# Kernel tuning notes

Measured on AMD Instinct MI355X. Metric: run time of the kernel, lower is better.

## Reference

```python
import jax, jax.numpy as jnp
import numpy as np

D_MODEL = 256
D_STATE = 256
BATCH = 32
SEQ = 4096
RMIN, RMAX = 0.9, 0.999
NEG_SLOPE = 0.01
EPS = 1e-5


def layer_norm(x, w=None, b=None):
    m = jnp.mean(x, axis=-1, keepdims=True)
    v = jnp.var(x, axis=-1, keepdims=True)
    y = (x - m) * jax.lax.rsqrt(v + EPS)
    if w is not None:
        y = y * w + b
    return y


def leaky_relu(x):
    return jnp.where(x >= 0, x, NEG_SLOPE * x)


def setup_inputs() -> dict:
    key = jax.random.key(0)
    ks = jax.random.split(key, 12)
    x = jax.random.normal(ks[0], (BATCH, SEQ, D_MODEL), dtype=jnp.float32)
    # LRU ring init: |lambda| uniform in [rmin, rmax], phase uniform in [0, 2pi]
    u1 = jax.random.uniform(ks[1], (D_STATE,), dtype=jnp.float32)
    u2 = jax.random.uniform(ks[2], (D_STATE,), dtype=jnp.float32)
    nu_log = jnp.log(-0.5 * jnp.log(u1 * (RMAX**2 - RMIN**2) + RMIN**2))
    theta_log = jnp.log(2 * jnp.pi * u2)
    lam_mod = jnp.exp(-jnp.exp(nu_log))
    gamma_log = jnp.log(jnp.sqrt(1.0 - lam_mod**2))
    B_re = jax.random.normal(ks[3], (D_STATE, D_MODEL)) / np.sqrt(2 * D_MODEL)
    B_im = jax.random.normal(ks[4], (D_STATE, D_MODEL)) / np.sqrt(2 * D_MODEL)
    C_re = jax.random.normal(ks[5], (D_STATE, D_STATE)) / np.sqrt(D_STATE)
    C_im = jax.random.normal(ks[6], (D_STATE, D_STATE)) / np.sqrt(D_STATE)
    Dm = jax.random.normal(ks[7], (D_STATE, D_MODEL)) / np.sqrt(D_MODEL)
    Wl = jax.random.normal(ks[8], (D_MODEL, D_STATE)) / np.sqrt(D_STATE)
    bl = jax.random.normal(ks[9], (D_MODEL,)) * 0.02
    Wr = jax.random.normal(ks[10], (D_MODEL, D_STATE)) / np.sqrt(D_STATE)
    br = jax.random.normal(ks[11], (D_MODEL,)) * 0.02
    ones_m = jnp.ones((D_MODEL,), jnp.float32)
    zeros_m = jnp.zeros((D_MODEL,), jnp.float32)
    ones_s = jnp.ones((D_STATE,), jnp.float32)
    zeros_s = jnp.zeros((D_STATE,), jnp.float32)
    return {
        "x": x,
        "ln1_w": ones_m, "ln1_b": zeros_m,
        "nu_log": nu_log, "theta_log": theta_log, "gamma_log": gamma_log,
        "B_re": B_re, "B_im": B_im, "C_re": C_re, "C_im": C_im, "Dm": Dm,
        "ln2_w": ones_s, "ln2_b": zeros_s,
        "Wl": Wl, "bl": bl, "Wr": Wr, "br": br,
        "ln4_w": ones_m, "ln4_b": zeros_m,
    }


def reference(x, ln1_w, ln1_b, nu_log, theta_log, gamma_log, B_re, B_im,
              C_re, C_im, Dm, ln2_w, ln2_b, Wl, bl, Wr, br, ln4_w, ln4_b):
    # pre-norm + residual skip
    x1 = layer_norm(x, ln1_w, ln1_b)          # [B, T, d_model]
    skip = x1
    u = leaky_relu(x1)
    # LRU: h_t = lambda * h_{t-1} + gamma * (B u_t); y = Re(C h) + D u
    lam_mod = jnp.exp(-jnp.exp(nu_log))
    theta = jnp.exp(theta_log)
    lr = lam_mod * jnp.cos(theta)             # [N]
    li = lam_mod * jnp.sin(theta)
    gam = jnp.exp(gamma_log)
    bu_re = gam * jnp.einsum('btd,nd->btn', u, B_re)  # [B, T, N]
    bu_im = gam * jnp.einsum('btd,nd->btn', u, B_im)
    bu_re_t = jnp.swapaxes(bu_re, 0, 1)       # [T, B, N]
    bu_im_t = jnp.swapaxes(bu_im, 0, 1)

    def step(carry, inp):
        hr, hi = carry
        br_t, bi_t = inp
        hr2 = lr * hr - li * hi + br_t
        hi2 = lr * hi + li * hr + bi_t
        return (hr2, hi2), (hr2, hi2)

    h0 = (jnp.zeros((x.shape[0], lr.shape[0]), x.dtype),
          jnp.zeros((x.shape[0], lr.shape[0]), x.dtype))
    (hr_last, hi_last), (hr, hi) = jax.lax.scan(step, h0, (bu_re_t, bu_im_t))
    hr = jnp.swapaxes(hr, 0, 1)               # [B, T, N]
    hi = jnp.swapaxes(hi, 0, 1)
    y = (jnp.einsum('btn,mn->btm', hr, C_re)
         - jnp.einsum('btn,mn->btm', hi, C_im)
         + jnp.einsum('btd,md->btm', u, Dm))  # [B, T, d_state]
    # post-norm + nonlinearity
    y = leaky_relu(layer_norm(y, ln2_w, ln2_b))
    # gated bilinear MLP
    xl = layer_norm(y @ Wl.T + bl)            # no affine
    xr = layer_norm(y @ Wr.T + br)
    out = layer_norm(xl * xr, ln4_w, ln4_b) + skip
    return out
```

## Files before the change

kernel.cpp:

```cpp
#include <hip/hip_runtime.h>
#include <cstdint>
#include <cstddef>

#define DEV __device__ __forceinline__

typedef unsigned short u16;
typedef short short8 __attribute__((ext_vector_type(8)));
typedef float floatx4 __attribute__((ext_vector_type(4)));

constexpr int BB = 32;
constexpr int TT = 4096;
constexpr int RR = BB * TT;
constexpr int CH = 64;
constexpr int LC = TT / CH;

constexpr size_t OFF_LAM  = 0;
constexpr size_t OFF_LAML = 2048;
constexpr size_t OFF_GAM  = 4096;
constexpr size_t OFF_B1   = 8192;
constexpr size_t OFF_B2   = OFF_B1 + (size_t)512 * 256 * 2;
constexpr size_t OFF_B3   = OFF_B2 + (size_t)256 * 768 * 2;
constexpr size_t OFF_BIG  = 2ull << 20;
constexpr size_t SZB      = (size_t)RR * 256 * 2;

DEV float bf2f(u16 u) {
    unsigned int i = ((unsigned int)u) << 16;
    float f;
    __builtin_memcpy(&f, &i, 4);
    return f;
}
DEV u16 f2bf(float f) {
    unsigned int i;
    __builtin_memcpy(&i, &f, 4);
    i += 0x7fffu + ((i >> 16) & 1u);
    return (u16)(i >> 16);
}

DEV void gload16(const void* g, void* l) {
    __builtin_amdgcn_global_load_lds(
        (const __attribute__((address_space(1))) unsigned int*)g,
        (__attribute__((address_space(3))) unsigned int*)l, 16, 0, 0);
}

__global__ __launch_bounds__(256)
void k_setup(const float* __restrict__ nu_log, const float* __restrict__ theta_log,
             const float* __restrict__ gamma_log,
             const float* __restrict__ B_re, const float* __restrict__ B_im,
             const float* __restrict__ C_re, const float* __restrict__ C_im,
             const float* __restrict__ Dm,
             const float* __restrict__ Wl, const float* __restrict__ Wr,
             char* __restrict__ ws)
{
    float2* lam  = (float2*)(ws + OFF_LAM);
    float2* lamL = (float2*)(ws + OFF_LAML);
    float*  gam  = (float*)(ws + OFF_GAM);
    u16* B1 = (u16*)(ws + OFF_B1);
    u16* B2 = (u16*)(ws + OFF_B2);
    u16* B3 = (u16*)(ws + OFF_B3);
    int g = blockIdx.x * 256 + threadIdx.x;
    int stride = gridDim.x * 256;
    if (g < 256) {
        float mod = expf(-expf(nu_log[g]));
        float th  = expf(theta_log[g]);
        float lr = mod * cosf(th), li = mod * sinf(th);
        lam[g] = make_float2(lr, li);
        gam[g] = expf(gamma_log[g]);
        float pr = 1.f, pi = 0.f;
        for (int i = 0; i < LC; i++) { float nr = pr*lr - pi*li; pi = pr*li + pi*lr; pr = nr; }
        lamL[g] = make_float2(pr, pi);
    }
    for (int i = g; i < 512*256; i += stride) {
        int n = i >> 8, d = i & 255;
        B1[i] = f2bf(n < 256 ? B_re[n*256 + d] : B_im[(n-256)*256 + d]);
    }
    for (int i = g; i < 256*768; i += stride) {
        int m = i / 768, k = i - m*768;
        float v = (k < 256) ? C_re[m*256 + k]
                : (k < 512) ? -C_im[m*256 + (k-256)]
                            : Dm[m*256 + (k-512)];
        B2[i] = f2bf(v);
    }
    for (int i = g; i < 512*256; i += stride) {
        int n = i >> 8, d = i & 255;
        B3[i] = f2bf(n < 256 ? Wl[n*256 + d] : Wr[(n-256)*256 + d]);
    }
}

__global__ __launch_bounds__(256)
void k_ln1(const float* __restrict__ x, const float* __restrict__ w, const float* __restrict__ b,
           u16* __restrict__ u, u16* __restrict__ skip)
{
    const int wv = threadIdx.x >> 6, lane = threadIdx.x & 63;
    const size_t row = (size_t)blockIdx.x * 4 + wv;
    float4 v = ((const float4*)(x + row * 256))[lane];
    float s = v.x + v.y + v.z + v.w;
    float q = v.x*v.x + v.y*v.y + v.z*v.z + v.w*v.w;
    #pragma unroll
    for (int o = 32; o; o >>= 1) { s += __shfl_xor(s, o); q += __shfl_xor(q, o); }
    const float m  = s * (1.f/256.f);
    const float rs = rsqrtf(q * (1.f/256.f) - m*m + 1e-5f);
    const float4 wv4 = ((const float4*)w)[lane];
    const float4 bv4 = ((const float4*)b)[lane];
    float y0 = (v.x - m) * rs * wv4.x + bv4.x;
    float y1 = (v.y - m) * rs * wv4.y + bv4.y;
    float y2 = (v.z - m) * rs * wv4.z + bv4.z;
    float y3 = (v.w - m) * rs * wv4.w + bv4.w;
    ((ushort4*)(skip + row * 256))[lane] = make_ushort4(f2bf(y0), f2bf(y1), f2bf(y2), f2bf(y3));
    float u0 = y0 >= 0.f ? y0 : 0.01f * y0;
    float u1 = y1 >= 0.f ? y1 : 0.01f * y1;
    float u2 = y2 >= 0.f ? y2 : 0.01f * y2;
    float u3 = y3 >= 0.f ? y3 : 0.01f * y3;
    ((ushort4*)(u + row * 256))[lane] = make_ushort4(f2bf(u0), f2bf(u1), f2bf(u2), f2bf(u3));
}

template<int MODE>
__global__ __launch_bounds__(256)
void k_gemm(const u16* __restrict__ A0, const u16* __restrict__ A1, const u16* __restrict__ A2,
            const u16* __restrict__ Bmat, u16* __restrict__ O0, u16* __restrict__ O1,
            const float* __restrict__ p0, const float* __restrict__ p1)
{
    constexpr int NKT = (MODE == 2) ? 12 : 4;
    constexpr int SB  = (MODE == 2) ? 768 : 256;
    __shared__ alignas(16) u16 As[128 * 64];
    __shared__ alignas(16) u16 Bs[128 * 64];
    const int wid = threadIdx.x >> 6, lane = threadIdx.x & 63;
    const int rowbase = blockIdx.x * 128;
    const int ct = blockIdx.y;
    const u16* Bbase = Bmat + (size_t)ct * 128 * SB;
    floatx4 acc[4][4];
    #pragma unroll
    for (int i = 0; i < 4; i++)
        #pragma unroll
        for (int j = 0; j < 4; j++)
            acc[i][j] = (floatx4){0.f, 0.f, 0.f, 0.f};

    for (int kt = 0; kt < NKT; ++kt) {
        const u16* Asrc; int kofs;
        if (MODE == 2) {
            if (kt < 4)      { Asrc = A0; kofs = kt * 64; }
            else if (kt < 8) { Asrc = A1; kofs = (kt - 4) * 64; }
            else             { Asrc = A2; kofs = (kt - 8) * 64; }
        } else { Asrc = A0; kofs = kt * 64; }
        __syncthreads();
        #pragma unroll
        for (int i = 0; i < 4; i++) {
            int grp = wid * 4 + i;
            const u16* ga = Asrc + (size_t)(rowbase + grp*8 + (lane >> 3)) * 256 + kofs + (lane & 7) * 8;
            gload16(ga, (char*)As + grp * 1024);
            const u16* gb = Bbase + (size_t)(grp*8 + (lane >> 3)) * SB + kt * 64 + (lane & 7) * 8;
            gload16(gb, (char*)Bs + grp * 1024);
        }
        __syncthreads();
        const int wm = wid >> 1, wn = wid & 1;
        short8 af[2][4], bfr[2][4];
        #pragma unroll
        for (int kk = 0; kk < 2; kk++) {
            #pragma unroll
            for (int mi = 0; mi < 4; mi++)
                af[kk][mi] = *(const short8*)&As[(wm*64 + mi*16 + (lane & 15)) * 64 + kk*32 + ((lane >> 4) * 8)];
            #pragma unroll
            for (int ni = 0; ni < 4; ni++)
                bfr[kk][ni] = *(const short8*)&Bs[(wn*64 + ni*16 + (lane & 15)) * 64 + kk*32 + ((lane >> 4) * 8)];
        }
        #pragma unroll
        for (int mi = 0; mi < 4; mi++)
            #pragma unroll
            for (int ni = 0; ni < 4; ni++) {
                acc[mi][ni] = __builtin_amdgcn_mfma_f32_16x16x32_bf16(af[0][mi], bfr[0][ni], acc[mi][ni], 0, 0, 0);
                acc[mi][ni] = __builtin_amdgcn_mfma_f32_16x16x32_bf16(af[1][mi], bfr[1][ni], acc[mi][ni], 0, 0, 0);
            }
    }
    const int wm = wid >> 1, wn = wid & 1;
    #pragma unroll
    for (int mi = 0; mi < 4; mi++) {
        #pragma unroll
        for (int ni = 0; ni < 4; ni++) {
            const int cc = wn*64 + ni*16 + (lane & 15);
            const int n  = ct * 128 + cc;
            float scale = 1.f, badd = 0.f;
            u16* outp; int col;
            if (MODE == 1)      { outp = (n < 256) ? O0 : O1; col = n & 255; scale = p0[col]; }
            else if (MODE == 2) { outp = O0; col = n; }
            else                { outp = (n < 256) ? O0 : O1; col = n & 255; badd = (n < 256 ? p0 : p1)[col]; }
            #pragma unroll
            for (int r = 0; r < 4; r++) {
                const int row = rowbase + wm*64 + mi*16 + ((lane >> 4) << 2) + r;
                float v = acc[mi][ni][r] * scale + badd;
                outp[(size_t)row * 256 + col] = f2bf(v);
            }
        }
    }
}

__global__ __launch_bounds__(128)
void k_scan1(const u16* __restrict__ bre, const u16* __restrict__ bim,
             float4* __restrict__ carry, const char* __restrict__ ws)
{
    const float2* lam = (const float2*)(ws + OFF_LAM);
    const int b = blockIdx.x, c = blockIdx.y, p = threadIdx.x;
    const unsigned int* pre = (const unsigned int*)bre;
    const unsigned int* pim = (const unsigned int*)bim;
    const float2 l0 = lam[2*p], l1 = lam[2*p + 1];
    float hr0 = 0, hi0 = 0, hr1 = 0, hi1 = 0;
    size_t base = ((size_t)b * TT + (size_t)c * LC) * 128 + p;
    #pragma unroll 8
    for (int j = 0; j < LC; j++) {
        unsigned int re = pre[base + (size_t)j * 128];
        unsigned int im = pim[base + (size_t)j * 128];
        float br0 = bf2f((u16)(re & 0xffff)), br1 = bf2f((u16)(re >> 16));
        float bi0 = bf2f((u16)(im & 0xffff)), bi1 = bf2f((u16)(im >> 16));
        float nr0 = fmaf(l0.x, hr0, fmaf(-l0.y, hi0, br0));
        float ni0 = fmaf(l0.x, hi0, fmaf( l0.y, hr0, bi0));
        float nr1 = fmaf(l1.x, hr1, fmaf(-l1.y, hi1, br1));
        float ni1 = fmaf(l1.x, hi1, fmaf( l1.y, hr1, bi1));
        hr0 = nr0; hi0 = ni0; hr1 = nr1; hi1 = ni1;
    }
    carry[((size_t)b * CH + c) * 128 + p] = make_float4(hr0, hi0, hr1, hi1);
}

__global__ __launch_bounds__(128)
void k_comb(float4* __restrict__ carry, const char* __restrict__ ws)
{
    const float2* lamL = (const float2*)(ws + OFF_LAML);
    const int b = blockIdx.x, p = threadIdx.x;
    const float2 L0 = lamL[2*p], L1 = lamL[2*p + 1];
    float4 prev = make_float4(0.f, 0.f, 0.f, 0.f);
    for (int c = 0; c < CH; c++) {
        size_t idx = ((size_t)b * CH + c) * 128 + p;
        float4 cur = carry[idx];
        carry[idx] = prev;
        float nx = fmaf(L0.x, prev.x, fmaf(-L0.y, prev.y, cur.x));
        float ny = fmaf(L0.x, prev.y, fmaf( L0.y, prev.x, cur.y));
        float nz = fmaf(L1.x, prev.z, fmaf(-L1.y, prev.w, cur.z));
        float nw = fmaf(L1.x, prev.w, fmaf( L1.y, prev.z, cur.w));
        prev = make_float4(nx, ny, nz, nw);
    }
}

__global__ __launch_bounds__(128)
void k_scan2(u16* __restrict__ bre, u16* __restrict__ bim,
             const float4* __restrict__ carry, const char* __restrict__ ws)
{
    const float2* lam = (const float2*)(ws + OFF_LAM);
    const int b = blockIdx.x, c = blockIdx.y, p = threadIdx.x;
    unsigned int* pre = (unsigned int*)bre;
    unsigned int* pim = (unsigned int*)bim;
    const float2 l0 = lam[2*p], l1 = lam[2*p + 1];
    float4 h0 = carry[((size_t)b * CH + c) * 128 + p];
    float hr0 = h0.x, hi0 = h0.y, hr1 = h0.z, hi1 = h0.w;
    size_t base = ((size_t)b * TT + (size_t)c * LC) * 128 + p;
    #pragma unroll 8
    for (int j = 0; j < LC; j++) {
        size_t idx = base + (size_t)j * 128;
        unsigned int re = pre[idx];
        unsigned int im = pim[idx];
        float br0 = bf2f((u16)(re & 0xffff)), br1 = bf2f((u16)(re >> 16));
        float bi0 = bf2f((u16)(im & 0xffff)), bi1 = bf2f((u16)(im >> 16));
        float nr0 = fmaf(l0.x, hr0, fmaf(-l0.y, hi0, br0));
        float ni0 = fmaf(l0.x, hi0, fmaf( l0.y, hr0, bi0));
        float nr1 = fmaf(l1.x, hr1, fmaf(-l1.y, hi1, br1));
        float ni1 = fmaf(l1.x, hi1, fmaf( l1.y, hr1, bi1));
        hr0 = nr0; hi0 = ni0; hr1 = nr1; hi1 = ni1;
        pre[idx] = ((unsigned int)f2bf(hr1) << 16) | f2bf(hr0);
        pim[idx] = ((unsigned int)f2bf(hi1) << 16) | f2bf(hi0);
    }
}

__global__ __launch_bounds__(256)
void k_ln2(u16* __restrict__ y, const float* __restrict__ w, const float* __restrict__ b)
{
    const int wv = threadIdx.x >> 6, lane = threadIdx.x & 63;
    const size_t row = (size_t)blockIdx.x * 4 + wv;
    ushort4 raw = ((const ushort4*)(y + row * 256))[lane];
    float v0 = bf2f(raw.x), v1 = bf2f(raw.y), v2 = bf2f(raw.z), v3 = bf2f(raw.w);
    float s = v0 + v1 + v2 + v3;
    float q = v0*v0 + v1*v1 + v2*v2 + v3*v3;
    #pragma unroll
    for (int o = 32; o; o >>= 1) { s += __shfl_xor(s, o); q += __shfl_xor(q, o); }
    const float m  = s * (1.f/256.f);
    const float rs = rsqrtf(q * (1.f/256.f) - m*m + 1e-5f);
    const float4 wv4 = ((const float4*)w)[lane];
    const float4 bv4 = ((const float4*)b)[lane];
    float y0 = (v0 - m) * rs * wv4.x + bv4.x;
    float y1 = (v1 - m) * rs * wv4.y + bv4.y;
    float y2 = (v2 - m) * rs * wv4.z + bv4.z;
    float y3 = (v3 - m) * rs * wv4.w + bv4.w;
    y0 = y0 >= 0.f ? y0 : 0.01f * y0;
    y1 = y1 >= 0.f ? y1 : 0.01f * y1;
    y2 = y2 >= 0.f ? y2 : 0.01f * y2;
    y3 = y3 >= 0.f ? y3 : 0.01f * y3;
    ((ushort4*)(y + row * 256))[lane] = make_ushort4(f2bf(y0), f2bf(y1), f2bf(y2), f2bf(y3));
}

__global__ __launch_bounds__(256)
void k_final(const u16* __restrict__ gl, const u16* __restrict__ gr, const u16* __restrict__ skip,
             const float* __restrict__ w4, const float* __restrict__ b4, float* __restrict__ out)
{
    const int wv = threadIdx.x >> 6, lane = threadIdx.x & 63;
    const size_t row = (size_t)blockIdx.x * 4 + wv;
    ushort4 ra = ((const ushort4*)(gl + row * 256))[lane];
    ushort4 rc = ((const ushort4*)(gr + row * 256))[lane];
    float a0 = bf2f(ra.x), a1 = bf2f(ra.y), a2 = bf2f(ra.z), a3 = bf2f(ra.w);
    float c0 = bf2f(rc.x), c1 = bf2f(rc.y), c2 = bf2f(rc.z), c3 = bf2f(rc.w);
    float s1 = a0+a1+a2+a3, q1 = a0*a0+a1*a1+a2*a2+a3*a3;
    float s2 = c0+c1+c2+c3, q2 = c0*c0+c1*c1+c2*c2+c3*c3;
    #pragma unroll
    for (int o = 32; o; o >>= 1) {
        s1 += __shfl_xor(s1, o); q1 += __shfl_xor(q1, o);
        s2 += __shfl_xor(s2, o); q2 += __shfl_xor(q2, o);
    }
    const float m1 = s1*(1.f/256.f), rs1 = rsqrtf(q1*(1.f/256.f) - m1*m1 + 1e-5f);
    const float m2 = s2*(1.f/256.f), rs2 = rsqrtf(q2*(1.f/256.f) - m2*m2 + 1e-5f);
    float v0 = ((a0-m1)*rs1) * ((c0-m2)*rs2);
    float v1 = ((a1-m1)*rs1) * ((c1-m2)*rs2);
    float v2 = ((a2-m1)*rs1) * ((c2-m2)*rs2);
    float v3 = ((a3-m1)*rs1) * ((c3-m2)*rs2);
    float s3 = v0+v1+v2+v3, q3 = v0*v0+v1*v1+v2*v2+v3*v3;
    #pragma unroll
    for (int o = 32; o; o >>= 1) { s3 += __shfl_xor(s3, o); q3 += __shfl_xor(q3, o); }
    const float m3 = s3*(1.f/256.f), rs3 = rsqrtf(q3*(1.f/256.f) - m3*m3 + 1e-5f);
    const float4 wv4 = ((const float4*)w4)[lane];
    const float4 bv4 = ((const float4*)b4)[lane];
    ushort4 sk = ((const ushort4*)(skip + row * 256))[lane];
    float o0 = (v0-m3)*rs3*wv4.x + bv4.x + bf2f(sk.x);
    float o1 = (v1-m3)*rs3*wv4.y + bv4.y + bf2f(sk.y);
    float o2 = (v2-m3)*rs3*wv4.z + bv4.z + bf2f(sk.z);
    float o3 = (v3-m3)*rs3*wv4.w + bv4.w + bf2f(sk.w);
    ((float4*)(out + row * 256))[lane] = make_float4(o0, o1, o2, o3);
}

extern "C" void kernel_launch(void* const* d_in, const int* in_sizes, int n_in,
                              void* d_out, int out_size, void* d_ws, size_t ws_size,
                              hipStream_t stream)
{
    (void)in_sizes; (void)n_in; (void)out_size; (void)ws_size;
    const float* x         = (const float*)d_in[0];
    const float* ln1_w     = (const float*)d_in[1];
    const float* ln1_b     = (const float*)d_in[2];
    const float* nu_log    = (const float*)d_in[3];
    const float* theta_log = (const float*)d_in[4];
    const float* gamma_log = (const float*)d_in[5];
    const float* B_re      = (const float*)d_in[6];
    const float* B_im      = (const float*)d_in[7];
    const float* C_re      = (const float*)d_in[8];
    const float* C_im      = (const float*)d_in[9];
    const float* Dm        = (const float*)d_in[10];
    const float* ln2_w     = (const float*)d_in[11];
    const float* ln2_b     = (const float*)d_in[12];
    const float* Wl        = (const float*)d_in[13];
    const float* bl        = (const float*)d_in[14];
    const float* Wr        = (const float*)d_in[15];
    const float* br        = (const float*)d_in[16];
    const float* ln4_w     = (const float*)d_in[17];
    const float* ln4_b     = (const float*)d_in[18];

    char* ws = (char*)d_ws;
    float* gam = (float*)(ws + OFF_GAM);
    u16* B1 = (u16*)(ws + OFF_B1);
    u16* B2 = (u16*)(ws + OFF_B2);
    u16* B3 = (u16*)(ws + OFF_B3);
    u16* u    = (u16*)(ws + OFF_BIG);
    u16* skip = (u16*)(ws + OFF_BIG + 1 * SZB);
    u16* bure = (u16*)(ws + OFF_BIG + 2 * SZB);
    u16* buim = (u16*)(ws + OFF_BIG + 3 * SZB);
    u16* y    = (u16*)(ws + OFF_BIG + 4 * SZB);
    float4* carry = (float4*)(ws + OFF_BIG + 5 * SZB);
    float* out = (float*)d_out;

    k_setup<<<dim3(256), dim3(256), 0, stream>>>(nu_log, theta_log, gamma_log,
                                                 B_re, B_im, C_re, C_im, Dm, Wl, Wr, ws);
    k_ln1<<<dim3(RR/4), dim3(256), 0, stream>>>(x, ln1_w, ln1_b, u, skip);
    k_gemm<1><<<dim3(RR/128, 4), dim3(256), 0, stream>>>(u, nullptr, nullptr, B1, bure, buim, gam, nullptr);
    k_scan1<<<dim3(BB, CH), dim3(128), 0, stream>>>(bure, buim, carry, ws);
    k_comb<<<dim3(BB), dim3(128), 0, stream>>>(carry, ws);
    k_scan2<<<dim3(BB, CH), dim3(128), 0, stream>>>(bure, buim, carry, ws);
    k_gemm<2><<<dim3(RR/128, 2), dim3(256), 0, stream>>>(bure, buim, u, B2, y, nullptr, nullptr, nullptr);
    k_ln2<<<dim3(RR/4), dim3(256), 0, stream>>>(y, ln2_w, ln2_b);
    k_gemm<3><<<dim3(RR/128, 4), dim3(256), 0, stream>>>(y, nullptr, nullptr, B3, bure, buim, bl, br);
    k_final<<<dim3(RR/4), dim3(256), 0, stream>>>(bure, buim, skip, ln4_w, ln4_b, out);
}
```

Measured before the change: 439.4 us.

## Double-buffer GEMM LDS tiles with XOR swizzle and prefetch carry loads

The GEMM kernel now keeps two LDS buffers and issues the global-to-LDS loads for the next k-tile before computing the current one, waiting with a partial vmcnt so memory traffic overlaps MFMA work. The LDS layout is XOR-swizzled by row to reduce bank conflicts on the short8 fragment reads. The carry-combine kernel also software-prefetches the next chunk's carry. The cost is twice the LDS per block, which may lower occupancy, and the hand-written vmcnt counts depend on gload16 issuing exactly one vm op per call.

Result: no change. 438.7 us (-0.2%).

```diff
diff --git a/kernel.cpp b/kernel.cpp
--- a/kernel.cpp
+++ b/kernel.cpp
@@ -121,12 +121,16 @@
 {
     constexpr int NKT = (MODE == 2) ? 12 : 4;
     constexpr int SB  = (MODE == 2) ? 768 : 256;
-    __shared__ alignas(16) u16 As[128 * 64];
-    __shared__ alignas(16) u16 Bs[128 * 64];
+    __shared__ alignas(16) u16 As[2][128 * 64];
+    __shared__ alignas(16) u16 Bs[2][128 * 64];
     const int wid = threadIdx.x >> 6, lane = threadIdx.x & 63;
     const int rowbase = blockIdx.x * 128;
     const int ct = blockIdx.y;
     const u16* Bbase = Bmat + (size_t)ct * 128 * SB;
+
+    const int srow  = lane >> 3;
+    const int sslot = (lane & 7) ^ srow;
+
     floatx4 acc[4][4];
     #pragma unroll
     for (int i = 0; i < 4; i++)
@@ -134,33 +138,45 @@
         for (int j = 0; j < 4; j++)
             acc[i][j] = (floatx4){0.f, 0.f, 0.f, 0.f};
 
-    for (int kt = 0; kt < NKT; ++kt) {
+    auto stage = [&](int kt, int pb) {
         const u16* Asrc; int kofs;
         if (MODE == 2) {
             if (kt < 4)      { Asrc = A0; kofs = kt * 64; }
             else if (kt < 8) { Asrc = A1; kofs = (kt - 4) * 64; }
             else             { Asrc = A2; kofs = (kt - 8) * 64; }
         } else { Asrc = A0; kofs = kt * 64; }
-        __syncthreads();
         #pragma unroll
         for (int i = 0; i < 4; i++) {
             int grp = wid * 4 + i;
-            const u16* ga = Asrc + (size_t)(rowbase + grp*8 + (lane >> 3)) * 256 + kofs + (lane & 7) * 8;
-            gload16(ga, (char*)As + grp * 1024);
-            const u16* gb = Bbase + (size_t)(grp*8 + (lane >> 3)) * SB + kt * 64 + (lane & 7) * 8;
-            gload16(gb, (char*)Bs + grp * 1024);
+            int row = grp * 8 + srow;
+            gload16(Asrc + (size_t)(rowbase + row) * 256 + kofs + sslot * 8,
+                    (char*)&As[pb][0] + grp * 1024);
+            gload16(Bbase + (size_t)row * SB + kt * 64 + sslot * 8,
+                    (char*)&Bs[pb][0] + grp * 1024);
         }
-        __syncthreads();
-        const int wm = wid >> 1, wn = wid & 1;
+    };
+
+    stage(0, 0);
+    const int wm = wid >> 1, wn = wid & 1;
+    for (int kt = 0; kt < NKT; ++kt) {
+        const int pb = kt & 1;
+        if (kt + 1 < NKT) {
+            stage(kt + 1, pb ^ 1);
+            asm volatile("s_waitcnt vmcnt(8)" ::: "memory");
+        } else {
+            asm volatile("s_waitcnt vmcnt(0)" ::: "memory");
+        }
+        __builtin_amdgcn_s_barrier();
         short8 af[2][4], bfr[2][4];
         #pragma unroll
         for (int kk = 0; kk < 2; kk++) {
+            const int rslot = (kk * 4 + (lane >> 4)) ^ (lane & 7);
             #pragma unroll
             for (int mi = 0; mi < 4; mi++)
-                af[kk][mi] = *(const short8*)&As[(wm*64 + mi*16 + (lane & 15)) * 64 + kk*32 + ((lane >> 4) * 8)];
+                af[kk][mi] = *(const short8*)&As[pb][(wm*64 + mi*16 + (lane & 15)) * 64 + rslot * 8];
             #pragma unroll
             for (int ni = 0; ni < 4; ni++)
-                bfr[kk][ni] = *(const short8*)&Bs[(wn*64 + ni*16 + (lane & 15)) * 64 + kk*32 + ((lane >> 4) * 8)];
+                bfr[kk][ni] = *(const short8*)&Bs[pb][(wn*64 + ni*16 + (lane & 15)) * 64 + rslot * 8];
         }
         #pragma unroll
         for (int mi = 0; mi < 4; mi++)
@@ -169,8 +185,9 @@
                 acc[mi][ni] = __builtin_amdgcn_mfma_f32_16x16x32_bf16(af[0][mi], bfr[0][ni], acc[mi][ni], 0, 0, 0);
                 acc[mi][ni] = __builtin_amdgcn_mfma_f32_16x16x32_bf16(af[1][mi], bfr[1][ni], acc[mi][ni], 0, 0, 0);
             }
-    }
-    const int wm = wid >> 1, wn = wid & 1;
+        __builtin_amdgcn_s_barrier();
+    }
+
     #pragma unroll
     for (int mi = 0; mi < 4; mi++) {
         #pragma unroll
@@ -225,10 +242,12 @@
     const int b = blockIdx.x, p = threadIdx.x;
     const float2 L0 = lamL[2*p], L1 = lamL[2*p + 1];
     float4 prev = make_float4(0.f, 0.f, 0.f, 0.f);
+    size_t base = (size_t)b * CH * 128 + p;
+    float4 nxt = carry[base];
     for (int c = 0; c < CH; c++) {
-        size_t idx = ((size_t)b * CH + c) * 128 + p;
-        float4 cur = carry[idx];
-        carry[idx] = prev;
+        float4 cur = nxt;
+        if (c + 1 < CH) nxt = carry[base + (size_t)(c + 1) * 128];
+        carry[base + (size_t)c * 128] = prev;
         float nx = fmaf(L0.x, prev.x, fmaf(-L0.y, prev.y, cur.x));
         float ny = fmaf(L0.x, prev.y, fmaf( L0.y, prev.x, cur.y));
         float nz = fmaf(L1.x, prev.z, fmaf(-L1.y, prev.w, cur.z));
```
